# Performance work log

Measured on AMD Instinct MI355X. Metric: run time of the kernel, lower is better.

Reference implementation:

```python
import jax, jax.numpy as jnp
import numpy as np


def conv1x1(x, W, b):
    # x: [B, C, H, W], W: [O, C], b: [O] -> [B, O, H, W]
    return jnp.einsum('bchw,oc->bohw', x, W) + b[None, :, None, None]


def setup_inputs() -> dict:
    key = jax.random.key(0)
    ks = jax.random.split(key, 8)
    B, C, H, W = 8, 128, 64, 64
    d = C // 8
    s = 0.05
    return {
        'x': jax.random.normal(ks[0], (B, C, H, W), jnp.float32),
        'Wq': jax.random.normal(ks[1], (d, C), jnp.float32) * s,
        'bq': jax.random.normal(ks[2], (d,), jnp.float32) * s,
        'Wk': jax.random.normal(ks[3], (d, C), jnp.float32) * s,
        'bk': jax.random.normal(ks[4], (d,), jnp.float32) * s,
        'Wv': jax.random.normal(ks[5], (C, C), jnp.float32) * s,
        'bv': jax.random.normal(ks[6], (C,), jnp.float32) * s,
        'gamma': jax.random.normal(ks[7], (1,), jnp.float32),
    }


def reference(x, Wq, bq, Wk, bk, Wv, bv, gamma):
    B, C, H, W = x.shape
    N = H * W
    q = conv1x1(x, Wq, bq).reshape(B, -1, N)      # [B, d, N]
    k = conv1x1(x, Wk, bk).reshape(B, -1, N)      # [B, d, N]
    v = conv1x1(x, Wv, bv).reshape(B, C, N)       # [B, C, N]
    # energy[b, i, j] = q_i . k_j  (no scaling, as in original)
    energy = jnp.einsum('bdi,bdj->bij', q, k)     # [B, N, N]
    attn = jax.nn.softmax(energy, axis=-1)
    # out[b, c, i] = sum_j v[b, c, j] * attn[b, i, j]
    out = jnp.einsum('bcj,bij->bci', v, attn).reshape(B, C, H, W)
    return gamma[0] * out + x
```

## Files before the change

kernel.cpp:

```cpp
#include <hip/hip_runtime.h>

#define BATCH 8
#define CCH   128
#define DQK   16
#define HW    4096
#define LOG2E 1.44269504088896340736f

typedef __attribute__((ext_vector_type(8))) short bf16x8;
typedef __attribute__((ext_vector_type(4))) float f32x4;

__device__ __forceinline__ unsigned cvt_pk_bf16(float lo, float hi) {
    unsigned r;
    asm("v_cvt_pk_bf16_f32 %0, %1, %2" : "=v"(r) : "v"(lo), "v"(hi));
    return r;
}

__device__ __forceinline__ void glds16(const void* gsrc, const void* lds) {
    auto* g = (const __attribute__((address_space(1))) unsigned int*)(unsigned long long)(uintptr_t)gsrc;
    auto* s = (__attribute__((address_space(3))) unsigned int*)(unsigned int)(uintptr_t)lds;
    __builtin_amdgcn_global_load_lds(g, s, 16, 0, 0);
}

__global__ __launch_bounds__(256) void qkv_kernel(
    const float* __restrict__ x,
    const float* __restrict__ Wq, const float* __restrict__ bq,
    const float* __restrict__ Wk, const float* __restrict__ bk,
    const float* __restrict__ Wv, const float* __restrict__ bv,
    ushort* __restrict__ qT, ushort* __restrict__ kT, ushort* __restrict__ v)
{
    const int blk = blockIdx.x;
    const int b   = blk >> 6;
    const int p0  = (blk & 63) << 6;
    const int t   = threadIdx.x;
    const int l   = t & 63;
    const int w   = t >> 6;
    const int lm  = l & 15;
    const int lg  = l >> 4;

    __shared__ __align__(16) ushort xT_l[64 * 136];

#pragma unroll
    for (int it = 0; it < 4; it++) {
        const int oc = w + 4 * it;
        float xr[8];
#pragma unroll
        for (int r = 0; r < 8; r++)
            xr[r] = x[((size_t)(b * CCH + oc * 8 + r)) * HW + p0 + l];
        unsigned u[4];
#pragma unroll
        for (int r = 0; r < 4; r++) u[r] = cvt_pk_bf16(xr[2 * r], xr[2 * r + 1]);
        *(bf16x8*)&xT_l[l * 136 + oc * 8] = *(bf16x8*)u;
    }
    __syncthreads();

    bf16x8 bfrag[4];
#pragma unroll
    for (int ks = 0; ks < 4; ks++)
        bfrag[ks] = *(const bf16x8*)&xT_l[(w * 16 + lm) * 136 + ks * 32 + lg * 8];

    f32x4 acc[10];
#pragma unroll
    for (int ot = 0; ot < 10; ot++)
#pragma unroll
        for (int r = 0; r < 4; r++) acc[ot][r] = 0.f;

#pragma unroll
    for (int ot = 0; ot < 10; ot++) {
        const float* Wrow;
        if (ot == 0)      Wrow = Wq + lm * CCH;
        else if (ot == 1) Wrow = Wk + lm * CCH;
        else              Wrow = Wv + (ot * 16 - 32 + lm) * CCH;
        const float scale = (ot == 0) ? LOG2E : 1.f;
#pragma unroll
        for (int ks = 0; ks < 4; ks++) {
            const float4 wa = *(const float4*)(Wrow + ks * 32 + lg * 8);
            const float4 wb = *(const float4*)(Wrow + ks * 32 + lg * 8 + 4);
            unsigned u[4];
            u[0] = cvt_pk_bf16(wa.x * scale, wa.y * scale);
            u[1] = cvt_pk_bf16(wa.z * scale, wa.w * scale);
            u[2] = cvt_pk_bf16(wb.x * scale, wb.y * scale);
            u[3] = cvt_pk_bf16(wb.z * scale, wb.w * scale);
            const bf16x8 afrag = *(bf16x8*)u;
            acc[ot] = __builtin_amdgcn_mfma_f32_16x16x32_bf16(afrag, bfrag[ks], acc[ot], 0, 0, 0);
        }
    }

    const int px = p0 + w * 16 + lm;
#pragma unroll
    for (int ot = 0; ot < 10; ot++) {
        const int ob = ot * 16 + 4 * lg;
        float4 bb;
        if (ot == 0) {
            bb = *(const float4*)(bq + 4 * lg);
            bb.x *= LOG2E; bb.y *= LOG2E; bb.z *= LOG2E; bb.w *= LOG2E;
        } else if (ot == 1) {
            bb = *(const float4*)(bk + 4 * lg);
        } else {
            bb = *(const float4*)(bv + (ot - 2) * 16 + 4 * lg);
        }
        const float r0 = acc[ot][0] + bb.x, r1 = acc[ot][1] + bb.y;
        const float r2 = acc[ot][2] + bb.z, r3 = acc[ot][3] + bb.w;
        const unsigned w0 = cvt_pk_bf16(r0, r1), w1 = cvt_pk_bf16(r2, r3);
        if (ot == 0) {
            uint2 pk; pk.x = w0; pk.y = w1;
            *(uint2*)&qT[((size_t)(b * HW + px)) * DQK + ob] = pk;
        } else if (ot == 1) {
            uint2 pk; pk.x = w0; pk.y = w1;
            *(uint2*)&kT[((size_t)(b * HW + px)) * DQK + (ob - 16)] = pk;
        } else {
            const int c = ob - 32;
            v[((size_t)(b * CCH + c + 0)) * HW + px] = (ushort)(w0 & 0xffff);
            v[((size_t)(b * CCH + c + 1)) * HW + px] = (ushort)(w0 >> 16);
            v[((size_t)(b * CCH + c + 2)) * HW + px] = (ushort)(w1 & 0xffff);
            v[((size_t)(b * CCH + c + 3)) * HW + px] = (ushort)(w1 >> 16);
        }
    }
}

__global__ __launch_bounds__(256) void attn_kernel(
    const ushort* __restrict__ qT, const ushort* __restrict__ kTg,
    const ushort* __restrict__ vg, const float* __restrict__ x,
    const float* __restrict__ gamma, float* __restrict__ out)
{
    const int blk = ((blockIdx.x & 7) << 6) | (blockIdx.x >> 3);
    const int b   = blk >> 6;
    const int i0  = (blk & 63) << 6;
    const int t   = threadIdx.x;
    const int l   = t & 63;
    const int w   = t >> 6;
    const int lm  = l & 15;
    const int lg  = l >> 4;

    __shared__ __align__(16) ushort kT_l[128 * 16];
    __shared__ __align__(16) ushort v_l [128 * 128];
    __shared__ __align__(16) ushort P_l [64 * 128];

    const ushort* kT_src = kTg + ((size_t)b * HW) * DQK + t * 8;
    ushort*       kT_dst = &kT_l[t * 8];
    const ushort* v_src[8];
    ushort*       v_dst[8];
#pragma unroll
    for (int it = 0; it < 8; it++) {
        const int idx = t + 256 * it;
        const int c   = idx >> 4;
        const int gs  = (idx & 15) ^ (c & 15);
        v_src[it] = vg + ((size_t)(b * CCH + c)) * HW + gs * 8;
        v_dst[it] = &v_l[idx * 8];
    }

    bf16x8 qf;
#pragma unroll
    for (int z = 0; z < 8; z++) qf[z] = 0;
    if (lg < 2)
        qf = *(const bf16x8*)(qT + ((size_t)(b * HW + i0 + 16 * w + lm)) * DQK + lg * 8);

    f32x4 zero4;
#pragma unroll
    for (int z = 0; z < 4; z++) zero4[z] = 0.f;

    f32x4 acc[8];
#pragma unroll
    for (int ct = 0; ct < 8; ct++) acc[ct] = zero4;

    float m_i = -1e30f, l_i = 0.f;

    for (int j0 = 0; j0 < HW; j0 += 128) {
        __syncthreads();

        glds16(kT_src + (size_t)j0 * DQK, kT_dst);
#pragma unroll
        for (int it = 0; it < 8; it++)
            glds16(v_src[it] + j0, v_dst[it]);
        __syncthreads();

        f32x4 s[8];
#pragma unroll
        for (int jt = 0; jt < 8; jt++) {
            bf16x8 kf = {};
            if (lg < 2)
                kf = *(const bf16x8*)&kT_l[(jt * 16 + lm) * 16 + lg * 8];
            s[jt] = __builtin_amdgcn_mfma_f32_16x16x32_bf16(kf, qf, zero4, 0, 0, 0);
        }

        float mx = s[0][0];
#pragma unroll
        for (int jt = 0; jt < 8; jt++)
#pragma unroll
            for (int r = 0; r < 4; r++) mx = fmaxf(mx, s[jt][r]);
        mx = fmaxf(mx, __shfl_xor(mx, 16));
        mx = fmaxf(mx, __shfl_xor(mx, 32));

        float m_new, alpha;
        if (__all(mx - m_i <= 8.f)) {
            m_new = m_i; alpha = 1.f;
        } else {
            m_new = fmaxf(m_i, mx);
            alpha = exp2f(m_i - m_new);
#pragma unroll
            for (int ct = 0; ct < 8; ct++) acc[ct] *= alpha;
        }

        float sum = 0.f;
        const int prow = (16 * w + lm) * 128;
#pragma unroll
        for (int jt = 0; jt < 8; jt++) {
            const float p0f = exp2f(s[jt][0] - m_new);
            const float p1f = exp2f(s[jt][1] - m_new);
            const float p2f = exp2f(s[jt][2] - m_new);
            const float p3f = exp2f(s[jt][3] - m_new);
            sum += (p0f + p1f) + (p2f + p3f);
            uint2 pk;
            pk.x = cvt_pk_bf16(p0f, p1f);
            pk.y = cvt_pk_bf16(p2f, p3f);
            const int g = (2 * jt + (lg >> 1)) ^ lm;
            *(uint2*)&P_l[prow + g * 8 + (lg & 1) * 4] = pk;
        }
        sum += __shfl_xor(sum, 16);
        sum += __shfl_xor(sum, 32);
        l_i = l_i * alpha + sum;
        m_i = m_new;

        __builtin_amdgcn_s_setprio(1);
#pragma unroll
        for (int ks = 0; ks < 4; ks++) {
            const int g = (4 * ks + lg) ^ lm;
            const bf16x8 pf = *(const bf16x8*)&P_l[prow + g * 8];
#pragma unroll
            for (int ct = 0; ct < 8; ct++) {
                const bf16x8 vf = *(const bf16x8*)&v_l[(ct * 16 + lm) * 128 + g * 8];
                acc[ct] = __builtin_amdgcn_mfma_f32_16x16x32_bf16(vf, pf, acc[ct], 0, 0, 0);
            }
        }
        __builtin_amdgcn_s_setprio(0);
    }

    const float linv = 1.f / l_i;
    const float gm = gamma[0];
    const int i = 16 * w + lm;
#pragma unroll
    for (int ct = 0; ct < 8; ct++) {
#pragma unroll
        for (int r = 0; r < 4; r++) {
            const int c = ct * 16 + lg * 4 + r;
            const size_t off = ((size_t)(b * CCH + c)) * HW + i0 + i;
            out[off] = gm * (acc[ct][r] * linv) + x[off];
        }
    }
}

extern "C" void kernel_launch(void* const* d_in, const int* in_sizes, int n_in,
                              void* d_out, int out_size, void* d_ws, size_t ws_size,
                              hipStream_t stream)
{
    const float* x     = (const float*)d_in[0];
    const float* Wq    = (const float*)d_in[1];
    const float* bq    = (const float*)d_in[2];
    const float* Wk    = (const float*)d_in[3];
    const float* bk    = (const float*)d_in[4];
    const float* Wv    = (const float*)d_in[5];
    const float* bv    = (const float*)d_in[6];
    const float* gamma = (const float*)d_in[7];
    float* out = (float*)d_out;

    ushort* qT = (ushort*)d_ws;
    ushort* kT = qT + (size_t)BATCH * HW * DQK;
    ushort* v  = kT + (size_t)BATCH * HW * DQK;

    qkv_kernel<<<dim3(BATCH * (HW / 64)), dim3(256), 0, stream>>>(
        x, Wq, bq, Wk, bk, Wv, bv, qT, kT, v);
    attn_kernel<<<dim3(BATCH * (HW / 64)), dim3(256), 0, stream>>>(
        qT, kT, v, x, gamma, out);
}
```

Before: 187.8 us.

## Pre-convert QKV weights to padded bf16 and pad kT rows in LDS

Adds a prep kernel that converts Wq/Wk/Wv to bf16 once, folds the log2e scale into Wq, and stores the rows padded to a stride of 136. The qkv kernel then streams these weights into LDS with global_load_lds and reads its MFMA A-fragments from there, instead of each wave loading fp32 weights and converting them. Separately, kT rows are padded from 16 to 24 elements in global memory and in LDS, which is meant to cut LDS bank conflicts on the kf fragment reads. In exchange there is an extra kernel launch, more LDS in qkv_kernel, and about 50% more kT bytes to load per tile, now split over two load instructions.

```diff
diff --git a/kernel.cpp b/kernel.cpp
--- a/kernel.cpp
+++ b/kernel.cpp
@@ -5,6 +5,9 @@
 #define DQK   16
 #define HW    4096
 #define LOG2E 1.44269504088896340736f
+#define KTS   24
+#define WTS   136
+#define WGRAN 2816
 
 typedef __attribute__((ext_vector_type(8))) short bf16x8;
 typedef __attribute__((ext_vector_type(4))) float f32x4;
@@ -21,11 +24,30 @@
     __builtin_amdgcn_global_load_lds(g, s, 16, 0, 0);
 }
 
+__global__ __launch_bounds__(256) void prep_kernel(
+    const float* __restrict__ Wq, const float* __restrict__ Wk,
+    const float* __restrict__ Wv, ushort* __restrict__ Wpad)
+{
+    const int idx = blockIdx.x * 256 + threadIdx.x;
+    if (idx >= 160 * (WTS / 2)) return;
+    const int row = idx / (WTS / 2);
+    const int c0  = (idx % (WTS / 2)) * 2;
+    unsigned val = 0;
+    if (c0 < CCH) {
+        const float* src;
+        float sc = 1.f;
+        if (row < 16)       { src = Wq + row * CCH;        sc = LOG2E; }
+        else if (row < 32)  { src = Wk + (row - 16) * CCH; }
+        else                { src = Wv + (row - 32) * CCH; }
+        val = cvt_pk_bf16(src[c0] * sc, src[c0 + 1] * sc);
+    }
+    *(unsigned*)&Wpad[row * WTS + c0] = val;
+}
+
 __global__ __launch_bounds__(256) void qkv_kernel(
-    const float* __restrict__ x,
-    const float* __restrict__ Wq, const float* __restrict__ bq,
-    const float* __restrict__ Wk, const float* __restrict__ bk,
-    const float* __restrict__ Wv, const float* __restrict__ bv,
+    const float* __restrict__ x, const ushort* __restrict__ Wpad,
+    const float* __restrict__ bq, const float* __restrict__ bk,
+    const float* __restrict__ bv,
     ushort* __restrict__ qT, ushort* __restrict__ kT, ushort* __restrict__ v)
 {
     const int blk = blockIdx.x;
@@ -37,7 +59,14 @@
     const int lm  = l & 15;
     const int lg  = l >> 4;
 
-    __shared__ __align__(16) ushort xT_l[64 * 136];
+    __shared__ __align__(16) ushort W_l[WGRAN * 8];
+    __shared__ __align__(16) ushort xT_l[64 * WTS];
+
+#pragma unroll
+    for (int i = 0; i < 11; i++) {
+        const int idx = t + 256 * i;
+        glds16(Wpad + idx * 8, &W_l[idx * 8]);
+    }
 
 #pragma unroll
     for (int it = 0; it < 4; it++) {
@@ -49,14 +78,14 @@
         unsigned u[4];
 #pragma unroll
         for (int r = 0; r < 4; r++) u[r] = cvt_pk_bf16(xr[2 * r], xr[2 * r + 1]);
-        *(bf16x8*)&xT_l[l * 136 + oc * 8] = *(bf16x8*)u;
+        *(bf16x8*)&xT_l[l * WTS + oc * 8] = *(bf16x8*)u;
     }
     __syncthreads();
 
     bf16x8 bfrag[4];
 #pragma unroll
     for (int ks = 0; ks < 4; ks++)
-        bfrag[ks] = *(const bf16x8*)&xT_l[(w * 16 + lm) * 136 + ks * 32 + lg * 8];
+        bfrag[ks] = *(const bf16x8*)&xT_l[(w * 16 + lm) * WTS + ks * 32 + lg * 8];
 
     f32x4 acc[10];
 #pragma unroll
@@ -66,21 +95,9 @@
 
 #pragma unroll
     for (int ot = 0; ot < 10; ot++) {
-        const float* Wrow;
-        if (ot == 0)      Wrow = Wq + lm * CCH;
-        else if (ot == 1) Wrow = Wk + lm * CCH;
-        else              Wrow = Wv + (ot * 16 - 32 + lm) * CCH;
-        const float scale = (ot == 0) ? LOG2E : 1.f;
 #pragma unroll
         for (int ks = 0; ks < 4; ks++) {
-            const float4 wa = *(const float4*)(Wrow + ks * 32 + lg * 8);
-            const float4 wb = *(const float4*)(Wrow + ks * 32 + lg * 8 + 4);
-            unsigned u[4];
-            u[0] = cvt_pk_bf16(wa.x * scale, wa.y * scale);
-            u[1] = cvt_pk_bf16(wa.z * scale, wa.w * scale);
-            u[2] = cvt_pk_bf16(wb.x * scale, wb.y * scale);
-            u[3] = cvt_pk_bf16(wb.z * scale, wb.w * scale);
-            const bf16x8 afrag = *(bf16x8*)u;
+            const bf16x8 afrag = *(const bf16x8*)&W_l[(ot * 16 + lm) * WTS + ks * 32 + lg * 8];
             acc[ot] = __builtin_amdgcn_mfma_f32_16x16x32_bf16(afrag, bfrag[ks], acc[ot], 0, 0, 0);
         }
     }
@@ -106,7 +123,7 @@
             *(uint2*)&qT[((size_t)(b * HW + px)) * DQK + ob] = pk;
         } else if (ot == 1) {
             uint2 pk; pk.x = w0; pk.y = w1;
-            *(uint2*)&kT[((size_t)(b * HW + px)) * DQK + (ob - 16)] = pk;
+            *(uint2*)&kT[((size_t)(b * HW + px)) * KTS + (ob - 16)] = pk;
         } else {
             const int c = ob - 32;
             v[((size_t)(b * CCH + c + 0)) * HW + px] = (ushort)(w0 & 0xffff);
@@ -131,12 +148,14 @@
     const int lm  = l & 15;
     const int lg  = l >> 4;
 
-    __shared__ __align__(16) ushort kT_l[128 * 16];
+    __shared__ __align__(16) ushort kT_l[128 * KTS];
     __shared__ __align__(16) ushort v_l [128 * 128];
     __shared__ __align__(16) ushort P_l [64 * 128];
 
-    const ushort* kT_src = kTg + ((size_t)b * HW) * DQK + t * 8;
-    ushort*       kT_dst = &kT_l[t * 8];
+    const ushort* kT_src0 = kTg + ((size_t)b * HW) * KTS + t * 8;
+    const ushort* kT_src1 = kTg + ((size_t)b * HW) * KTS + (256 + t) * 8;
+    ushort*       kT_dst0 = &kT_l[t * 8];
+    ushort*       kT_dst1 = &kT_l[(256 + t) * 8];
     const ushort* v_src[8];
     ushort*       v_dst[8];
 #pragma unroll
@@ -167,7 +186,9 @@
     for (int j0 = 0; j0 < HW; j0 += 128) {
         __syncthreads();
 
-        glds16(kT_src + (size_t)j0 * DQK, kT_dst);
+        glds16(kT_src0 + (size_t)j0 * KTS, kT_dst0);
+        if (t < 128)
+            glds16(kT_src1 + (size_t)j0 * KTS, kT_dst1);
 #pragma unroll
         for (int it = 0; it < 8; it++)
             glds16(v_src[it] + j0, v_dst[it]);
@@ -178,7 +199,7 @@
         for (int jt = 0; jt < 8; jt++) {
             bf16x8 kf = {};
             if (lg < 2)
-                kf = *(const bf16x8*)&kT_l[(jt * 16 + lm) * 16 + lg * 8];
+                kf = *(const bf16x8*)&kT_l[(jt * 16 + lm) * KTS + lg * 8];
             s[jt] = __builtin_amdgcn_mfma_f32_16x16x32_bf16(kf, qf, zero4, 0, 0, 0);
         }
 
@@ -262,12 +283,14 @@
     const float* gamma = (const float*)d_in[7];
     float* out = (float*)d_out;
 
-    ushort* qT = (ushort*)d_ws;
-    ushort* kT = qT + (size_t)BATCH * HW * DQK;
-    ushort* v  = kT + (size_t)BATCH * HW * DQK;
-
+    ushort* qT   = (ushort*)d_ws;
+    ushort* kT   = qT + (size_t)BATCH * HW * DQK;
+    ushort* v    = kT + (size_t)BATCH * HW * KTS;
+    ushort* Wpad = v  + (size_t)BATCH * CCH * HW;
+
+    prep_kernel<<<dim3(43), dim3(256), 0, stream>>>(Wq, Wk, Wv, Wpad);
     qkv_kernel<<<dim3(BATCH * (HW / 64)), dim3(256), 0, stream>>>(
-        x, Wq, bq, Wk, bk, Wv, bv, qT, kT, v);
+        x, Wpad, bq, bk, bv, qT, kT, v);
     attn_kernel<<<dim3(BATCH * (HW / 64)), dim3(256), 0, stream>>>(
         qT, kT, v, x, gamma, out);
 }
```

New measurement: 173.5 us. -7.6%, faster.
